# Kernel tuning notes

Hardware: AMD Instinct MI355X
Metric: run time of the kernel (lower is better)

## Reference

```python
import jax, jax.numpy as jnp
import numpy as np

SIGNAL_DIM = 64   # D
STATE_DIM = 64    # N
SEQ_LEN = 16384   # L
BATCH = 16


def _init_dplr_hippo(state_dim):
    """NumPy port of init_DPLR_HiPPO(signal_dim=1, state_dim). Returns Lambda,(N,) P,(N,) B,(N,1) complex64."""
    n = np.arange(state_dim, dtype=np.float64)
    A = np.zeros((state_dim, state_dim))
    for k in range(state_dim):
        A[k:, k] = np.sqrt(2.0 * np.arange(k, state_dim) + 1.0) * np.sqrt(2.0 * k + 1.0)
        A[k, k] = k + 1
    A = -A
    P = np.sqrt(n + 0.5)
    SI = A + P[:, None] * P[None, :]
    diag = np.diagonal(SI).copy()
    S = SI - np.diag(diag)
    eigvals, V = np.linalg.eigh(S * -1j)   # S*-1j is Hermitian
    Lam = diag + 1j * eigvals
    Vc = V.conj().T
    Pc = Vc @ P.astype(np.complex128)
    B = np.sqrt(2.0 * n + 1.0)[:, None]    # (N, 1): signal_dim=1, tied across channels
    Bc = Vc @ B.astype(np.complex128)
    return Lam.astype(np.complex64), Pc.astype(np.complex64), Bc.astype(np.complex64)


def _ri(x):
    # complex -> (..., 2) float32, matching torch.view_as_real parameter storage
    return jnp.stack([jnp.real(x), jnp.imag(x)], axis=-1).astype(jnp.float32)


def _to_c(x):
    return jax.lax.complex(x[..., 0], x[..., 1])


def setup_inputs() -> dict:
    key = jax.random.key(0)
    ku, kc1, kc2, kd, ks = jax.random.split(key, 5)
    Lam, P, B = _init_dplr_hippo(STATE_DIM)
    C = (jax.random.normal(kc1, (SIGNAL_DIM, STATE_DIM)) +
         1j * jax.random.normal(kc2, (SIGNAL_DIM, STATE_DIM))).astype(jnp.complex64)
    return {
        "u": jax.random.normal(ku, (BATCH, SEQ_LEN, SIGNAL_DIM), dtype=jnp.float32),
        "Lambda_ri": _ri(jnp.asarray(Lam)),      # (N, 2)
        "P_ri": _ri(jnp.asarray(P)),             # (N, 2)
        "B_ri": _ri(jnp.asarray(B)),             # (N, 1, 2)
        "C_ri": _ri(C),                          # (D, N, 2)
        "D_param": jax.random.normal(kd, (SIGNAL_DIM,), dtype=jnp.float32),
        "log_step": jnp.log(jax.random.uniform(ks, (1,), minval=0.001, maxval=0.1)).astype(jnp.float32),
    }


def reference(u, Lambda_ri, P_ri, B_ri, C_ri, D_param, log_step):
    Lam = _to_c(Lambda_ri)   # (N,)
    P = _to_c(P_ri)          # (N,)
    B = _to_c(B_ri)          # (N, 1)
    C = _to_c(C_ri)          # (D, N)
    L = u.shape[-2]

    step = jnp.exp(log_step)                                  # (1,)
    Omega = jnp.exp(-2j * jnp.pi * (jnp.arange(L) / L))       # (L,) roots of unity
    g = (2.0 / step) * ((1.0 - Omega) / (1.0 + Omega))        # (L,)

    # Batched Cauchy kernel: k_ab[l] = sum_n a_n * b_n / (g_l - Lambda_n)
    cauchy = 1.0 / (g[:, None] - Lam[None, :])                # (L, N)
    a0 = jnp.conj(C)        # (D, N)
    a1 = jnp.conj(P)        # (N,)
    b0 = B[:, 0]            # (N,)  == B.T row (signal_dim=1)
    b1 = P                  # (N,)
    k00 = jnp.einsum('dn,n,ln->dl', a0, b0, cauchy)
    k01 = jnp.einsum('dn,n,ln->dl', a0, b1, cauchy)
    k10 = jnp.einsum('n,n,ln->l', a1, b0, cauchy)
    k11 = jnp.einsum('n,n,ln->l', a1, b1, cauchy)

    evaluated = (2.0 / (1.0 + Omega)) * (k00 - k01 * (1.0 / (1.0 + k11)) * k10)  # (D, L)
    K = jnp.fft.ifft(evaluated, axis=-1).T.real               # (L, D) conv kernel

    # FFT convolution along time axis (zero-pad to 2L, linear convolution)
    ud = jnp.fft.rfft(jnp.pad(u, ((0, 0), (0, L), (0, 0))), axis=-2)
    Kd = jnp.fft.rfft(jnp.pad(K, ((0, L), (0, 0))), axis=-2)
    y = jnp.fft.irfft(ud * Kd, n=2 * L, axis=-2)[..., :L, :]
    return y + D_param * u
```

## Files before the change

### kernel.cpp

```cpp
#include <hip/hip_runtime.h>
#include <math.h>

#define MF 16384
#define HALF 8192

__device__ __forceinline__ float2 cmul(float2 a, float2 b){ return make_float2(a.x*b.x - a.y*b.y, a.x*b.y + a.y*b.x); }
__device__ __forceinline__ float2 cmulc(float2 a, float2 b){ return make_float2(a.x*b.x + a.y*b.y, a.y*b.x - a.x*b.y); }
__device__ __forceinline__ int rho4(int v){ return ((v & 3) << 2) | (v >> 2); }
__device__ __forceinline__ int sob(int k){
    return (rho4(k & 15) << 10) | (rho4((k >> 4) & 15) << 6) | (rho4((k >> 8) & 15) << 2) | (k >> 12);
}
__device__ __forceinline__ int ph(int e){ return e ^ ((e >> 4) & 3) ^ (((e >> 6) & 3) << 2); }

__device__ __forceinline__ void bf4f(float2&a,float2&b,float2&c,float2&d){
    float t0x=a.x+c.x, t0y=a.y+c.y, t2x=a.x-c.x, t2y=a.y-c.y;
    float t1x=b.x+d.x, t1y=b.y+d.y, t3x=b.x-d.x, t3y=b.y-d.y;
    a=make_float2(t0x+t1x,t0y+t1y);
    b=make_float2(t2x+t3y,t2y-t3x);
    c=make_float2(t0x-t1x,t0y-t1y);
    d=make_float2(t2x-t3y,t2y+t3x);
}
__device__ __forceinline__ void bf4i(float2&a,float2&b,float2&c,float2&d){
    float t0x=a.x+c.x, t0y=a.y+c.y, t2x=a.x-c.x, t2y=a.y-c.y;
    float t1x=b.x+d.x, t1y=b.y+d.y, t3x=b.x-d.x, t3y=b.y-d.y;
    a=make_float2(t0x+t1x,t0y+t1y);
    b=make_float2(t2x-t3y,t2y+t3x);
    c=make_float2(t0x-t1x,t0y-t1y);
    d=make_float2(t2x+t3y,t2y-t3x);
}

#define W16_1 make_float2(0.92387953251128674f, -0.38268343236508978f)
#define W16_2 make_float2(0.70710678118654752f, -0.70710678118654752f)
#define W16_3 make_float2(0.38268343236508978f, -0.92387953251128674f)
#define W16_6 make_float2(-0.70710678118654752f, -0.70710678118654752f)
#define W16_9 make_float2(-0.92387953251128674f, 0.38268343236508978f)

__device__ __forceinline__ void dft16_fwd(float2* x){
    bf4f(x[0],x[4],x[8],x[12]);
    bf4f(x[1],x[5],x[9],x[13]);
    bf4f(x[2],x[6],x[10],x[14]);
    bf4f(x[3],x[7],x[11],x[15]);
    x[5]=cmul(x[5],W16_1);  x[9]=cmul(x[9],W16_2);   x[13]=cmul(x[13],W16_3);
    x[6]=cmul(x[6],W16_2);  { float2 t=x[10]; x[10]=make_float2(t.y,-t.x); } x[14]=cmul(x[14],W16_6);
    x[7]=cmul(x[7],W16_3);  x[11]=cmul(x[11],W16_6); x[15]=cmul(x[15],W16_9);
    bf4f(x[0],x[1],x[2],x[3]);
    bf4f(x[4],x[5],x[6],x[7]);
    bf4f(x[8],x[9],x[10],x[11]);
    bf4f(x[12],x[13],x[14],x[15]);
}
__device__ __forceinline__ void dft16_inv(float2* x){
    bf4i(x[0],x[1],x[2],x[3]);
    bf4i(x[4],x[5],x[6],x[7]);
    bf4i(x[8],x[9],x[10],x[11]);
    bf4i(x[12],x[13],x[14],x[15]);
    x[5]=cmulc(x[5],W16_1); x[9]=cmulc(x[9],W16_2);  x[13]=cmulc(x[13],W16_3);
    x[6]=cmulc(x[6],W16_2); { float2 t=x[10]; x[10]=make_float2(-t.y,t.x); } x[14]=cmulc(x[14],W16_6);
    x[7]=cmulc(x[7],W16_3); x[11]=cmulc(x[11],W16_6); x[15]=cmulc(x[15],W16_9);
    bf4i(x[0],x[4],x[8],x[12]);
    bf4i(x[1],x[5],x[9],x[13]);
    bf4i(x[2],x[6],x[10],x[14]);
    bf4i(x[3],x[7],x[11],x[15]);
}

template<bool INV>
__device__ __forceinline__ void tw0_apply(float2* x, float2 w1){
    float2 w2=cmul(w1,w1), w4=cmul(w2,w2), w8=cmul(w4,w4);
    float2 w3=cmul(w2,w1), w5=cmul(w4,w1), w6=cmul(w4,w2), w7=cmul(w4,w3);
    float2 w9=cmul(w8,w1), w10=cmul(w8,w2), w11=cmul(w8,w3), w12=cmul(w8,w4);
    float2 w13=cmul(w8,w5), w14=cmul(w8,w6), w15=cmul(w8,w7);
    if (!INV){
        x[1]=cmul(x[1],w4);   x[2]=cmul(x[2],w8);   x[3]=cmul(x[3],w12);
        x[4]=cmul(x[4],w1);   x[5]=cmul(x[5],w5);   x[6]=cmul(x[6],w9);
        x[7]=cmul(x[7],w13);  x[8]=cmul(x[8],w2);   x[9]=cmul(x[9],w6);
        x[10]=cmul(x[10],w10);x[11]=cmul(x[11],w14);x[12]=cmul(x[12],w3);
        x[13]=cmul(x[13],w7); x[14]=cmul(x[14],w11);x[15]=cmul(x[15],w15);
    } else {
        x[1]=cmulc(x[1],w4);   x[2]=cmulc(x[2],w8);   x[3]=cmulc(x[3],w12);
        x[4]=cmulc(x[4],w1);   x[5]=cmulc(x[5],w5);   x[6]=cmulc(x[6],w9);
        x[7]=cmulc(x[7],w13);  x[8]=cmulc(x[8],w2);   x[9]=cmulc(x[9],w6);
        x[10]=cmulc(x[10],w10);x[11]=cmulc(x[11],w14);x[12]=cmulc(x[12],w3);
        x[13]=cmulc(x[13],w7); x[14]=cmulc(x[14],w11);x[15]=cmulc(x[15],w15);
    }
}

template<bool INV>
__device__ __forceinline__ void pass0(float2* A, float2 w1g, int tid){
    float2 x[16];
    int base = ph(tid);
    #pragma unroll
    for(int m=0;m<16;++m) x[m] = A[base + (m<<10)];
    if(!INV){ dft16_fwd(x); tw0_apply<false>(x, w1g); }
    else { tw0_apply<true>(x, w1g); dft16_inv(x); }
    #pragma unroll
    for(int m=0;m<16;++m) A[base + (m<<10)] = x[m];
}

template<bool INV>
__device__ __forceinline__ void pass1(float2* A, const float2* tw1s, int tid){
    float2 x[16];
    int i1 = tid & 63;
    int B = (tid >> 6) << 10;
    int i1x = i1 ^ ((i1 >> 4) & 3);
    int b0 = B | i1x;
    int b1 = B | 64 | (i1x ^ 4);
    int b2 = B | 128 | (i1x ^ 8);
    int b3 = B | 192 | (i1x ^ 12);
    x[0]=A[b0];     x[1]=A[b1];     x[2]=A[b2];     x[3]=A[b3];
    x[4]=A[b0+256]; x[5]=A[b1+256]; x[6]=A[b2+256]; x[7]=A[b3+256];
    x[8]=A[b0+512]; x[9]=A[b1+512]; x[10]=A[b2+512];x[11]=A[b3+512];
    x[12]=A[b0+768];x[13]=A[b1+768];x[14]=A[b2+768];x[15]=A[b3+768];
    if(!INV){
        dft16_fwd(x);
        #pragma unroll
        for(int j=1;j<16;++j) x[j] = cmul(x[j], tw1s[(j<<6)+i1]);
    } else {
        #pragma unroll
        for(int j=1;j<16;++j) x[j] = cmulc(x[j], tw1s[(j<<6)+i1]);
        dft16_inv(x);
    }
    A[b0]=x[0];     A[b1]=x[1];     A[b2]=x[2];     A[b3]=x[3];
    A[b0+256]=x[4]; A[b1+256]=x[5]; A[b2+256]=x[6]; A[b3+256]=x[7];
    A[b0+512]=x[8]; A[b1+512]=x[9]; A[b0==b0?b2+512:0]=x[10];A[b3+512]=x[11];
    A[b0+768]=x[12];A[b1+768]=x[13];A[b2+768]=x[14];A[b3+768]=x[15];
}

template<bool INV>
__device__ __forceinline__ void pass2(float2* A, const float2* tw2s, int tid){
    float2 x[16];
    int q = tid >> 2, j2 = tid & 3;
    int qb = q << 6, qa = q & 3;
    int c0 = qb | (j2 ^ 0);
    int c1 = qb | 16 | (j2 ^ 1);
    int c2 = qb | 32 | (j2 ^ 2);
    int c3 = qb | 48 | (j2 ^ 3);
    int r0 = (qa ^ 0) << 2, r1 = (qa ^ 1) << 2, r2 = (qa ^ 2) << 2, r3 = (qa ^ 3) << 2;
    x[0]=A[c0+r0];  x[1]=A[c0+r1];  x[2]=A[c0+r2];  x[3]=A[c0+r3];
    x[4]=A[c1+r0];  x[5]=A[c1+r1];  x[6]=A[c1+r2];  x[7]=A[c1+r3];
    x[8]=A[c2+r0];  x[9]=A[c2+r1];  x[10]=A[c2+r2]; x[11]=A[c2+r3];
    x[12]=A[c3+r0]; x[13]=A[c3+r1]; x[14]=A[c3+r2]; x[15]=A[c3+r3];
    if(!INV){
        dft16_fwd(x);
        #pragma unroll
        for(int j=1;j<16;++j) x[j] = cmul(x[j], tw2s[(j<<2)+j2]);
    } else {
        #pragma unroll
        for(int j=1;j<16;++j) x[j] = cmulc(x[j], tw2s[(j<<2)+j2]);
        dft16_inv(x);
    }
    A[c0+r0]=x[0];  A[c0+r1]=x[1];  A[c0+r2]=x[2];  A[c0+r3]=x[3];
    A[c1+r0]=x[4];  A[c1+r1]=x[5];  A[c1+r2]=x[6];  A[c1+r3]=x[7];
    A[c2+r0]=x[8];  A[c2+r1]=x[9];  A[c2+r2]=x[10]; A[c2+r3]=x[11];
    A[c3+r0]=x[12]; A[c3+r1]=x[13]; A[c3+r2]=x[14]; A[c3+r3]=x[15];
}

template<bool INV>
__device__ __forceinline__ void pass3(float2* A, int tid){
    int sgm = ((tid>>2)&3) ^ (((tid>>4)&3)<<2);
    #pragma unroll
    for(int rr=0; rr<4; ++rr){
        int base = (tid<<2) | (rr<<12);
        float2 a=A[(base|0)^sgm], b=A[(base|1)^sgm], c=A[(base|2)^sgm], d=A[(base|3)^sgm];
        if(!INV) bf4f(a,b,c,d); else bf4i(a,b,c,d);
        A[(base|0)^sgm]=a; A[(base|1)^sgm]=b; A[(base|2)^sgm]=c; A[(base|3)^sgm]=d;
    }
}

__global__ __launch_bounds__(1024) void k_evalinit(const float2* __restrict__ Lam, const float2* __restrict__ P,
        const float2* __restrict__ Bc, const float2* __restrict__ C,
        const float* __restrict__ log_step, float2* __restrict__ E,
        float2* __restrict__ baseg, float2* __restrict__ tw1g, float2* __restrict__ tw2g) {
    __shared__ float2 bTs[16][64];
    __shared__ float2 pTs[16][64];
    __shared__ float2 S10s[16], S11s[16];
    __shared__ float2 C_l[64][65];
    __shared__ float2 tile[16][65];
    int tid = threadIdx.x;
    if (blockIdx.x >= 256){
        const double TP = 6.2831853071795864769;
        double a = -TP * (double)tid / 16384.0;
        baseg[tid] = make_float2((float)cos(a), (float)sin(a));
        double a1 = -TP * (double)((tid & 63) * rho4(tid >> 6)) / 1024.0;
        tw1g[tid] = make_float2((float)cos(a1), (float)sin(a1));
        if (tid < 64){
            double a2 = -TP * (double)((tid & 3) * rho4(tid >> 2)) / 64.0;
            tw2g[tid] = make_float2((float)cos(a2), (float)sin(a2));
        }
        return;
    }
    int l0 = blockIdx.x * 64;
    float step = expf(log_step[0]);
    {
        int dq = tid >> 6, n = tid & 63;
        #pragma unroll
        for (int p = 0; p < 4; ++p) { int dd = dq + p * 16; C_l[n][dd] = C[dd * 64 + n]; }
    }
    __syncthreads();
    int w = tid >> 6;
    int lane = tid & 63;
    for (int p = 0; p < 4; ++p) {
        int l = l0 + p * 16 + w;
        float lf = (float)l * (1.0f / 16384.0f);
        float s2 = sinpif(lf), c2 = cospif(lf);
        float2 q1 = make_float2(2.0f*c2*c2, -2.0f*s2*c2);
        {
            int n = lane;
            float2 q2 = make_float2(4.0f*s2*s2, 4.0f*s2*c2);
            float2 ln = Lam[n];
            float2 lq = cmul(ln, q1);
            float2 den = make_float2(q2.x - step*lq.x, q2.y - step*lq.y);
            float idn = step / (den.x*den.x + den.y*den.y);
            float2 T = make_float2(den.x*idn, -den.y*idn);
            float2 bn = Bc[n], pn = P[n];
            float2 bT = cmul(bn, T), pT = cmul(pn, T);
            bTs[w][n] = bT; pTs[w][n] = pT;
            float2 s10 = make_float2(pn.x*bT.x + pn.y*bT.y, pn.x*bT.y - pn.y*bT.x);
            float2 s11 = make_float2(pn.x*pT.x + pn.y*pT.y, pn.x*pT.y - pn.y*pT.x);
            #pragma unroll
            for (int off = 32; off > 0; off >>= 1) {
                s10.x += __shfl_xor(s10.x, off);
                s10.y += __shfl_xor(s10.y, off);
                s11.x += __shfl_xor(s11.x, off);
                s11.y += __shfl_xor(s11.y, off);
            }
            if (n == 0) { S10s[w] = s10; S11s[w] = s11; }
        }
        __syncthreads();
        {
            int d = lane;
            float2 S00 = make_float2(0.f, 0.f), S01 = make_float2(0.f, 0.f);
            #pragma unroll 8
            for (int n = 0; n < 64; ++n) {
                float2 cn = C_l[n][d];
                float2 bT = bTs[w][n];
                float2 pT = pTs[w][n];
                S00.x += cn.x*bT.x + cn.y*bT.y;  S00.y += cn.x*bT.y - cn.y*bT.x;
                S01.x += cn.x*pT.x + cn.y*pT.y;  S01.y += cn.x*pT.y - cn.y*pT.x;
            }
            float2 S10 = S10s[w], S11 = S11s[w];
            float2 k11 = cmul(q1, S11); k11.x += 1.0f;
            float2 k10q = cmul(q1, S10);
            float ik = 1.0f / (k11.x*k11.x + k11.y*k11.y);
            float2 quo = make_float2((k10q.x*k11.x + k10q.y*k11.y) * ik,
                                     (k10q.y*k11.x - k10q.x*k11.y) * ik);
            float2 corr = cmul(S01, quo);
            tile[w][d] = make_float2(2.0f*(S00.x - corr.x), 2.0f*(S00.y - corr.y));
        }
        __syncthreads();
        {
            int lo = tid & 15, dq = tid >> 4;
            E[(size_t)dq * MF + l0 + p * 16 + lo] = tile[lo][dq];
        }
        __syncthreads();
    }
}

union MidShm {
    struct { float2 A[MF]; float2 tw1s[1024]; float2 tw2s[64]; } p;
    float t[256][65];
};

__global__ __launch_bounds__(1024)
__attribute__((amdgpu_waves_per_eu(4, 4)))
void k_mid(const float2* __restrict__ E, float4* __restrict__ Ktab,
        const float2* __restrict__ baseg, const float2* __restrict__ tw1g, const float2* __restrict__ tw2g,
        const float* __restrict__ u, float* __restrict__ uT) {
    __shared__ MidShm sh;
    int tid = threadIdx.x;
    if (blockIdx.x >= 64){
        int cid = blockIdx.x - 64;
        int b = cid >> 6, t0c = (cid & 63) << 8;
        const float* ub = u + ((size_t)(b * MF + t0c)) * 64;
        #pragma unroll
        for (int it = 0; it < 16; ++it){
            int tl = it * 16 + (tid >> 6), dl = tid & 63;
            sh.t[tl][dl] = ub[(size_t)tl * 64 + dl];
        }
        __syncthreads();
        float* dst = uT + (size_t)b * 64 * MF + t0c;
        #pragma unroll
        for (int it = 0; it < 16; ++it){
            int dd = (tid >> 8) + it * 4, tl = tid & 255;
            dst[(size_t)dd * MF + tl] = sh.t[tl][dd];
        }
        return;
    }
    float2* A = sh.p.A;
    float2* tw1s = sh.p.tw1s;
    float2* tw2s = sh.p.tw2s;
    float2 w1g = baseg[tid];
    tw1s[tid] = tw1g[tid];
    if (tid < 64) tw2s[tid] = tw2g[tid];
    int d = blockIdx.x;
    const float2* Ed = E + (size_t)d * MF;
    #pragma unroll
    for (int r = 0; r < 16; ++r) { int l = tid + (r << 10); A[ph(sob(l))] = Ed[l]; }
    __syncthreads();
    pass3<true>(A, tid); __syncthreads();
    pass2<true>(A, tw2s, tid); __syncthreads();
    pass1<true>(A, tw1s, tid); __syncthreads();
    pass0<true>(A, w1g, tid); __syncthreads();
    const float s = 1.0f / (float)MF;
    float2 rv[8];
    #pragma unroll
    for (int r = 0; r < 8; ++r) {
        int t = tid + (r << 10);
        rv[r] = make_float2(A[ph(2*t)].x * s, A[ph(2*t+1)].x * s);
    }
    __syncthreads();
    int pht = ph(tid);
    #pragma unroll
    for (int r = 0; r < 16; ++r) A[pht + (r << 10)] = (r < 8) ? rv[r] : make_float2(0.f, 0.f);
    __syncthreads();
    pass0<false>(A, w1g, tid); __syncthreads();
    pass1<false>(A, tw1s, tid); __syncthreads();
    pass2<false>(A, tw2s, tid); __syncthreads();
    pass3<false>(A, tid); __syncthreads();
    float4* Kd = Ktab + (size_t)d * MF;
    int Cbits = (rho4(tid >> 6) << 4) | (rho4((tid >> 2) & 15) << 8) | ((tid & 3) << 12);
    const float ksc = 1.0f / (float)MF;
    #pragma unroll
    for (int r = 0; r < 16; ++r) {
        int k = Cbits | rho4(r);
        int kp = (MF - k) & (MF - 1);
        int p = sob(kp);
        float kf = (float)k * (1.0f / 16384.0f);
        float2 w = make_float2(cospif(kf), -sinpif(kf));
        float2 Zk = A[pht + (r << 10)];
        float2 Zm = A[ph(p)]; Zm.y = -Zm.y;
        float2 Ue = make_float2(0.5f*(Zk.x + Zm.x), 0.5f*(Zk.y + Zm.y));
        float2 dd = make_float2(Zk.x - Zm.x, Zk.y - Zm.y);
        float2 Uo = make_float2(0.5f*dd.y, -0.5f*dd.x);
        float2 t2 = cmul(w, Uo);
        Kd[tid + (r << 10)] = make_float4((Ue.x + t2.x)*ksc, (Ue.y + t2.y)*ksc,
                                          (Ue.x - t2.x)*ksc, (Ue.y - t2.y)*ksc);
    }
}

template<bool TRANS>
__global__ __launch_bounds__(1024)
__attribute__((amdgpu_waves_per_eu(4, 4)))
void k_conv(const float* __restrict__ u, const float* __restrict__ uT,
        const float4* __restrict__ Ktab, const float* __restrict__ Dp,
        float* __restrict__ yT, float* __restrict__ yout,
        const float2* __restrict__ baseg, const float2* __restrict__ tw1g, const float2* __restrict__ tw2g) {
    __shared__ float2 A[MF];
    __shared__ float2 tw1s[1024];
    __shared__ float2 tw2s[64];
    int tid = threadIdx.x;
    float2 w1g = baseg[tid];
    tw1s[tid] = tw1g[tid];
    if (tid < 64) tw2s[tid] = tw2g[tid];
    int bid = blockIdx.x;
    int vb = ((bid & 7) << 7) | (bid >> 3);
    int d = vb >> 4, b = vb & 15;
    int bd = (b << 6) | d;
    int base = ph(tid);
    const float2* src = (const float2*)(uT + (size_t)bd * MF);
    const float* ub = u + ((size_t)b * MF) * 64 + d;
    {
        float2 x[16];
        #pragma unroll
        for (int m = 0; m < 16; ++m){
            if (m < 8){
                if (TRANS) x[m] = src[tid + (m << 10)];
                else { int t = tid + (m << 10); x[m] = make_float2(ub[(size_t)(2*t)*64], ub[(size_t)(2*t+1)*64]); }
            } else x[m] = make_float2(0.f, 0.f);
        }
        dft16_fwd(x);
        tw0_apply<false>(x, w1g);
        #pragma unroll
        for (int m = 0; m < 16; ++m) A[base + (m << 10)] = x[m];
    }
    __syncthreads();
    pass1<false>(A, tw1s, tid); __syncthreads();
    pass2<false>(A, tw2s, tid); __syncthreads();
    const float4* Kd = Ktab + (size_t)d * MF;
    float4 kd[16];
    #pragma unroll
    for (int r = 0; r < 16; ++r) kd[r] = Kd[tid + (r << 10)];
    pass3<false>(A, tid); __syncthreads();
    int Cbits = (rho4(tid >> 6) << 4) | (rho4((tid >> 2) & 15) << 8) | ((tid & 3) << 12);
    float2 Wr[16];
    #pragma unroll
    for (int r = 0; r < 16; ++r) {
        int k = Cbits | rho4(r);
        int kp = (MF - k) & (MF - 1);
        int p = sob(kp);
        float kf = (float)k * (1.0f / 16384.0f);
        float2 w = make_float2(cospif(kf), -sinpif(kf));
        float2 Zk = A[base + (r << 10)];
        float2 Zm = A[ph(p)]; Zm.y = -Zm.y;
        float2 Ue = make_float2(0.5f*(Zk.x + Zm.x), 0.5f*(Zk.y + Zm.y));
        float2 dd = make_float2(Zk.x - Zm.x, Zk.y - Zm.y);
        float2 Uo = make_float2(0.5f*dd.y, -0.5f*dd.x);
        float2 t2 = cmul(w, Uo);
        float2 X0 = make_float2(Ue.x + t2.x, Ue.y + t2.y);
        float2 X1 = make_float2(Ue.x - t2.x, Ue.y - t2.y);
        float2 Y0 = cmul(X0, make_float2(kd[r].x, kd[r].y));
        float2 Y1 = cmul(X1, make_float2(kd[r].z, kd[r].w));
        float2 Ey = make_float2(0.5f*(Y0.x + Y1.x), 0.5f*(Y0.y + Y1.y));
        float2 Dy = make_float2(Y0.x - Y1.x, Y0.y - Y1.y);
        float2 Oy = cmulc(Dy, w);
        Oy.x *= 0.5f; Oy.y *= 0.5f;
        Wr[r] = make_float2(Ey.x - Oy.y, Ey.y + Oy.x);
    }
    __syncthreads();
    #pragma unroll
    for (int r = 0; r < 16; ++r) A[base + (r << 10)] = Wr[r];
    __syncthreads();
    pass3<true>(A, tid); __syncthreads();
    pass2<true>(A, tw2s, tid); __syncthreads();
    pass1<true>(A, tw1s, tid); __syncthreads();
    {
        float2 x[16];
        #pragma unroll
        for (int m = 0; m < 16; ++m) x[m] = A[base + (m << 10)];
        tw0_apply<true>(x, w1g);
        dft16_inv(x);
        if (TRANS){
            float2* dst = (float2*)(yT + (size_t)bd * MF);
            #pragma unroll
            for (int m = 0; m < 8; ++m) dst[tid + (m << 10)] = x[m];
        } else {
            float Dd = Dp[d];
            float* yb = yout + ((size_t)b * MF) * 64 + d;
            #pragma unroll
            for (int m = 0; m < 8; ++m){
                int t = tid + (m << 10);
                yb[(size_t)(2*t)*64]   = x[m].x + Dd * ub[(size_t)(2*t)*64];
                yb[(size_t)(2*t+1)*64] = x[m].y + Dd * ub[(size_t)(2*t+1)*64];
            }
        }
    }
}

__global__ void k_out(const float* __restrict__ yT, const float* __restrict__ u,
                      const float* __restrict__ Dp, float* __restrict__ y) {
    __shared__ float tile[64][65];
    int b = blockIdx.y, t0 = blockIdx.x * 64, tid = threadIdx.x;
    #pragma unroll
    for (int k2 = 0; k2 < 16; ++k2) {
        int idx = tid + k2 * 256;
        int dl = idx >> 6, tl = idx & 63;
        tile[dl][tl] = yT[((size_t)b * 64 + dl) * MF + t0 + tl];
    }
    __syncthreads();
    #pragma unroll
    for (int k2 = 0; k2 < 16; ++k2) {
        int idx = tid + k2 * 256;
        int tl = idx >> 6, dl = idx & 63;
        size_t gi = ((size_t)(b * MF + t0 + tl)) * 64 + dl;
        y[gi] = tile[dl][tl] + Dp[dl] * u[gi];
    }
}

extern "C" void kernel_launch(void* const* d_in, const int* in_sizes, int n_in,
                              void* d_out, int out_size, void* d_ws, size_t ws_size,
                              hipStream_t stream) {
    const float*  u   = (const float*)d_in[0];
    const float2* Lam = (const float2*)d_in[1];
    const float2* P   = (const float2*)d_in[2];
    const float2* Bc  = (const float2*)d_in[3];
    const float2* C   = (const float2*)d_in[4];
    const float*  Dp  = (const float*)d_in[5];
    const float*  ls  = (const float*)d_in[6];
    float* y = (float*)d_out;
    char* ws = (char*)d_ws;

    size_t off = 0;
    float2* baseg = (float2*)(ws + off); off += (size_t)1024 * sizeof(float2);
    float2* tw1g  = (float2*)(ws + off); off += (size_t)1024 * sizeof(float2);
    float2* tw2g  = (float2*)(ws + off); off += (size_t)64 * sizeof(float2) + 512;
    float2* E     = (float2*)(ws + off); off += (size_t)64 * MF * sizeof(float2);
    float4* Ktab  = (float4*)(ws + off); off += (size_t)64 * MF * sizeof(float4);
    float*  uT    = (float*) (ws + off); off += (size_t)1024 * MF * sizeof(float);
    float*  yT    = (float*) (ws + off); off += (size_t)1024 * MF * sizeof(float);
    bool trans = (ws_size >= off);

    k_evalinit<<<257, 1024, 0, stream>>>(Lam, P, Bc, C, ls, E, baseg, tw1g, tw2g);
    k_mid<<<trans ? 1088 : 64, 1024, 0, stream>>>(E, Ktab, baseg, tw1g, tw2g, u, uT);

    if (trans) {
        k_conv<true><<<1024, 1024, 0, stream>>>(u, uT, Ktab, Dp, yT, y, baseg, tw1g, tw2g);
        k_out<<<dim3(MF / 64, 16), 256, 0, stream>>>(yT, u, Dp, y);
    } else {
        k_conv<false><<<1024, 1024, 0, stream>>>(u, nullptr, Ktab, Dp, nullptr, y, baseg, tw1g, tw2g);
    }
}
```

Baseline: 307.5 us.

## Cut register pressure in conv pointwise stage and drop forced waves-per-EU

The pointwise spectral multiply in k_conv now runs in five groups of rows, paired by mirror index, with a barrier before each group's writes. This replaces holding all 16 kernel float4 values and 16 results in registers at once, and the Ktab loads are no longer hoisted ahead of pass3. The twiddle computation in tw0_apply is rewritten as an incremental chain of products so fewer powers are live at once, and the amdgpu_waves_per_eu(4,4) attribute is removed from k_mid and k_conv. The goal is lower VGPR pressure and fewer spills, at the cost of extra barriers, global-load latency that is no longer hidden behind pass3, and slightly more rounding error from the chained twiddles.

```diff
diff --git a/kernel.cpp b/kernel.cpp
--- a/kernel.cpp
+++ b/kernel.cpp
@@ -64,22 +64,27 @@
 
 template<bool INV>
 __device__ __forceinline__ void tw0_apply(float2* x, float2 w1){
-    float2 w2=cmul(w1,w1), w4=cmul(w2,w2), w8=cmul(w4,w4);
-    float2 w3=cmul(w2,w1), w5=cmul(w4,w1), w6=cmul(w4,w2), w7=cmul(w4,w3);
-    float2 w9=cmul(w8,w1), w10=cmul(w8,w2), w11=cmul(w8,w3), w12=cmul(w8,w4);
-    float2 w13=cmul(w8,w5), w14=cmul(w8,w6), w15=cmul(w8,w7);
-    if (!INV){
-        x[1]=cmul(x[1],w4);   x[2]=cmul(x[2],w8);   x[3]=cmul(x[3],w12);
-        x[4]=cmul(x[4],w1);   x[5]=cmul(x[5],w5);   x[6]=cmul(x[6],w9);
-        x[7]=cmul(x[7],w13);  x[8]=cmul(x[8],w2);   x[9]=cmul(x[9],w6);
-        x[10]=cmul(x[10],w10);x[11]=cmul(x[11],w14);x[12]=cmul(x[12],w3);
-        x[13]=cmul(x[13],w7); x[14]=cmul(x[14],w11);x[15]=cmul(x[15],w15);
-    } else {
-        x[1]=cmulc(x[1],w4);   x[2]=cmulc(x[2],w8);   x[3]=cmulc(x[3],w12);
-        x[4]=cmulc(x[4],w1);   x[5]=cmulc(x[5],w5);   x[6]=cmulc(x[6],w9);
-        x[7]=cmulc(x[7],w13);  x[8]=cmulc(x[8],w2);   x[9]=cmulc(x[9],w6);
-        x[10]=cmulc(x[10],w10);x[11]=cmulc(x[11],w14);x[12]=cmulc(x[12],w3);
-        x[13]=cmulc(x[13],w7); x[14]=cmulc(x[14],w11);x[15]=cmulc(x[15],w15);
+    float2 w4;
+    { float2 w2 = cmul(w1,w1); w4 = cmul(w2,w2); }
+    {
+        float2 wc = w4;
+        if(!INV) x[1]=cmul(x[1],wc); else x[1]=cmulc(x[1],wc);
+        wc = cmul(wc,w4);
+        if(!INV) x[2]=cmul(x[2],wc); else x[2]=cmulc(x[2],wc);
+        wc = cmul(wc,w4);
+        if(!INV) x[3]=cmul(x[3],wc); else x[3]=cmulc(x[3],wc);
+    }
+    float2 wrow = w1;
+    #pragma unroll
+    for(int row=1; row<4; ++row){
+        float2 wc = wrow;
+        #pragma unroll
+        for(int c=0;c<4;++c){
+            int m = 4*row + c;
+            if(!INV) x[m]=cmul(x[m],wc); else x[m]=cmulc(x[m],wc);
+            if (c < 3) wc = cmul(wc,w4);
+        }
+        if (row < 3) wrow = cmul(wrow,w1);
     }
 }
 
@@ -120,7 +125,7 @@
     }
     A[b0]=x[0];     A[b1]=x[1];     A[b2]=x[2];     A[b3]=x[3];
     A[b0+256]=x[4]; A[b1+256]=x[5]; A[b2+256]=x[6]; A[b3+256]=x[7];
-    A[b0+512]=x[8]; A[b1+512]=x[9]; A[b0==b0?b2+512:0]=x[10];A[b3+512]=x[11];
+    A[b0+512]=x[8]; A[b1+512]=x[9]; A[b2+512]=x[10];A[b3+512]=x[11];
     A[b0+768]=x[12];A[b1+768]=x[13];A[b2+768]=x[14];A[b3+768]=x[15];
 }
 
@@ -163,6 +168,32 @@
         if(!INV) bf4f(a,b,c,d); else bf4i(a,b,c,d);
         A[(base|0)^sgm]=a; A[(base|1)^sgm]=b; A[(base|2)^sgm]=c; A[(base|3)^sgm]=d;
     }
+}
+
+template<int R>
+__device__ __forceinline__ float2 pw_compute(const float2* A, const float4* Kd,
+                                             int tid, int base, int Cbits){
+    constexpr int RR = ((R & 3) << 2) | (R >> 2);
+    int k = Cbits | RR;
+    int kp = (MF - k) & (MF - 1);
+    int p = sob(kp);
+    float kf = (float)k * (1.0f / 16384.0f);
+    float2 w = make_float2(cospif(kf), -sinpif(kf));
+    float2 Zk = A[base + (R << 10)];
+    float2 Zm = A[ph(p)]; Zm.y = -Zm.y;
+    float4 kr = Kd[tid + (R << 10)];
+    float2 Ue = make_float2(0.5f*(Zk.x + Zm.x), 0.5f*(Zk.y + Zm.y));
+    float2 dd = make_float2(Zk.x - Zm.x, Zk.y - Zm.y);
+    float2 Uo = make_float2(0.5f*dd.y, -0.5f*dd.x);
+    float2 t2 = cmul(w, Uo);
+    float2 X0 = make_float2(Ue.x + t2.x, Ue.y + t2.y);
+    float2 X1 = make_float2(Ue.x - t2.x, Ue.y - t2.y);
+    float2 Y0 = cmul(X0, make_float2(kr.x, kr.y));
+    float2 Y1 = cmul(X1, make_float2(kr.z, kr.w));
+    float2 Ey = make_float2(0.5f*(Y0.x + Y1.x), 0.5f*(Y0.y + Y1.y));
+    float2 Dy = make_float2(Y0.x - Y1.x, Y0.y - Y1.y);
+    float2 Oy = cmulc(Dy, w);
+    return make_float2(Ey.x - 0.5f*Oy.y, Ey.y + 0.5f*Oy.x);
 }
 
 __global__ __launch_bounds__(1024) void k_evalinit(const float2* __restrict__ Lam, const float2* __restrict__ P,
@@ -260,7 +291,6 @@
 };
 
 __global__ __launch_bounds__(1024)
-__attribute__((amdgpu_waves_per_eu(4, 4)))
 void k_mid(const float2* __restrict__ E, float4* __restrict__ Ktab,
         const float2* __restrict__ baseg, const float2* __restrict__ tw1g, const float2* __restrict__ tw2g,
         const float* __restrict__ u, float* __restrict__ uT) {
@@ -338,7 +368,6 @@
 
 template<bool TRANS>
 __global__ __launch_bounds__(1024)
-__attribute__((amdgpu_waves_per_eu(4, 4)))
 void k_conv(const float* __restrict__ u, const float* __restrict__ uT,
         const float4* __restrict__ Ktab, const float* __restrict__ Dp,
         float* __restrict__ yT, float* __restrict__ yout,
@@ -374,39 +403,50 @@
     __syncthreads();
     pass1<false>(A, tw1s, tid); __syncthreads();
     pass2<false>(A, tw2s, tid); __syncthreads();
-    const float4* Kd = Ktab + (size_t)d * MF;
-    float4 kd[16];
-    #pragma unroll
-    for (int r = 0; r < 16; ++r) kd[r] = Kd[tid + (r << 10)];
     pass3<false>(A, tid); __syncthreads();
-    int Cbits = (rho4(tid >> 6) << 4) | (rho4((tid >> 2) & 15) << 8) | ((tid & 3) << 12);
-    float2 Wr[16];
-    #pragma unroll
-    for (int r = 0; r < 16; ++r) {
-        int k = Cbits | rho4(r);
-        int kp = (MF - k) & (MF - 1);
-        int p = sob(kp);
-        float kf = (float)k * (1.0f / 16384.0f);
-        float2 w = make_float2(cospif(kf), -sinpif(kf));
-        float2 Zk = A[base + (r << 10)];
-        float2 Zm = A[ph(p)]; Zm.y = -Zm.y;
-        float2 Ue = make_float2(0.5f*(Zk.x + Zm.x), 0.5f*(Zk.y + Zm.y));
-        float2 dd = make_float2(Zk.x - Zm.x, Zk.y - Zm.y);
-        float2 Uo = make_float2(0.5f*dd.y, -0.5f*dd.x);
-        float2 t2 = cmul(w, Uo);
-        float2 X0 = make_float2(Ue.x + t2.x, Ue.y + t2.y);
-        float2 X1 = make_float2(Ue.x - t2.x, Ue.y - t2.y);
-        float2 Y0 = cmul(X0, make_float2(kd[r].x, kd[r].y));
-        float2 Y1 = cmul(X1, make_float2(kd[r].z, kd[r].w));
-        float2 Ey = make_float2(0.5f*(Y0.x + Y1.x), 0.5f*(Y0.y + Y1.y));
-        float2 Dy = make_float2(Y0.x - Y1.x, Y0.y - Y1.y);
-        float2 Oy = cmulc(Dy, w);
-        Oy.x *= 0.5f; Oy.y *= 0.5f;
-        Wr[r] = make_float2(Ey.x - Oy.y, Ey.y + Oy.x);
-    }
-    __syncthreads();
-    #pragma unroll
-    for (int r = 0; r < 16; ++r) A[base + (r << 10)] = Wr[r];
+    {
+        const float4* Kd = Ktab + (size_t)d * MF;
+        int Cbits = (rho4(tid >> 6) << 4) | (rho4((tid >> 2) & 15) << 8) | ((tid & 3) << 12);
+        {
+            float2 wa = pw_compute<0>(A, Kd, tid, base, Cbits);
+            float2 wb = pw_compute<2>(A, Kd, tid, base, Cbits);
+            __syncthreads();
+            A[base + (0<<10)] = wa; A[base + (2<<10)] = wb;
+        }
+        {
+            float2 wa = pw_compute<1>(A, Kd, tid, base, Cbits);
+            float2 wb = pw_compute<3>(A, Kd, tid, base, Cbits);
+            float2 wc = pw_compute<9>(A, Kd, tid, base, Cbits);
+            float2 wd = pw_compute<10>(A, Kd, tid, base, Cbits);
+            __syncthreads();
+            A[base + (1<<10)] = wa; A[base + (3<<10)] = wb;
+            A[base + (9<<10)] = wc; A[base + (10<<10)] = wd;
+        }
+        {
+            float2 wa = pw_compute<4>(A, Kd, tid, base, Cbits);
+            float2 wb = pw_compute<15>(A, Kd, tid, base, Cbits);
+            float2 wc = pw_compute<5>(A, Kd, tid, base, Cbits);
+            float2 wd = pw_compute<14>(A, Kd, tid, base, Cbits);
+            __syncthreads();
+            A[base + (4<<10)] = wa; A[base + (15<<10)] = wb;
+            A[base + (5<<10)] = wc; A[base + (14<<10)] = wd;
+        }
+        {
+            float2 wa = pw_compute<6>(A, Kd, tid, base, Cbits);
+            float2 wb = pw_compute<13>(A, Kd, tid, base, Cbits);
+            float2 wc = pw_compute<7>(A, Kd, tid, base, Cbits);
+            float2 wd = pw_compute<12>(A, Kd, tid, base, Cbits);
+            __syncthreads();
+            A[base + (6<<10)] = wa; A[base + (13<<10)] = wb;
+            A[base + (7<<10)] = wc; A[base + (12<<10)] = wd;
+        }
+        {
+            float2 wa = pw_compute<8>(A, Kd, tid, base, Cbits);
+            float2 wb = pw_compute<11>(A, Kd, tid, base, Cbits);
+            __syncthreads();
+            A[base + (8<<10)] = wa; A[base + (11<<10)] = wb;
+        }
+    }
     __syncthreads();
     pass3<true>(A, tid); __syncthreads();
     pass2<true>(A, tw2s, tid); __syncthreads();
```

New measurement: 293.2 us. 1.05x faster.
